# Kernel optimization log

Hardware: AMD Instinct MI355X
Metric: run time of the kernel (lower is better)

Reference implementation:

```python
import jax, jax.numpy as jnp
import numpy as np

N = 1_000_000
D_IN = 9      # 4 (pe) + 1 (q) + 4 (s)
D_H = 30      # dim_evolution
D_OUT = 1     # dim
SLOPE = 0.01  # torch LeakyReLU default negative_slope


def setup_inputs() -> dict:
    key = jax.random.key(0)
    ks = jax.random.split(key, 11)
    def lin(kw, kb, fan_in, fan_out):
        bound = 1.0 / np.sqrt(fan_in)
        W = jax.random.uniform(kw, (fan_in, fan_out), jnp.float32, -bound, bound)
        b = jax.random.uniform(kb, (fan_out,), jnp.float32, -bound, bound)
        return W, b
    W1, b1 = lin(ks[0], ks[1], D_IN, D_H)
    W2, b2 = lin(ks[2], ks[3], D_H, D_H)
    W3, b3 = lin(ks[4], ks[5], D_H, D_H)
    W4, b4 = lin(ks[6], ks[7], D_H, D_OUT)
    return {
        "input_pe": jax.random.normal(ks[8], (N, 4), jnp.float32),
        "input_q": jax.random.normal(ks[9], (N, 1), jnp.float32),
        "input_s": jax.random.normal(ks[10], (N, 4), jnp.float32),
        "W1": W1, "b1": b1, "W2": W2, "b2": b2,
        "W3": W3, "b3": b3, "W4": W4, "b4": b4,
    }


def reference(input_pe, input_q, input_s, W1, b1, W2, b2, W3, b3, W4, b4):
    # forward MLP 9->30->30->30->1 with LeakyReLU
    x = jnp.concatenate([input_pe, input_q, input_s], axis=1)  # [N,9]
    z1 = x @ W1 + b1
    h1 = jnp.where(z1 > 0, z1, SLOPE * z1)
    z2 = h1 @ W2 + b2
    h2 = jnp.where(z2 > 0, z2, SLOPE * z2)
    z3 = h2 @ W3 + b3
    h3 = jnp.where(z3 > 0, z3, SLOPE * z3)
    out = h3 @ W4 + b4  # [N,1]

    # analytic per-sample gradient of scalar output wrt the 9 inputs
    # (equivalent to torch.autograd.grad with grad_outputs=ones)
    gz3 = W4[:, 0][None, :] * jnp.where(z3 > 0, 1.0, SLOPE)  # [N,30]
    gz2 = (gz3 @ W3.T) * jnp.where(z2 > 0, 1.0, SLOPE)       # [N,30]
    gz1 = (gz2 @ W2.T) * jnp.where(z1 > 0, 1.0, SLOPE)       # [N,30]
    gx = gz1 @ W1.T                                           # [N,9]

    n = x.shape[0]
    h_pe = gx[:, 0:4].reshape(n, 1, 4)
    h_q = gx[:, 4:5].reshape(n, 1, 1)
    h_s = gx[:, 5:9].reshape(n, 1, 4)
    return (out, h_s, h_q, h_pe)
```

## Files before the change

### kernel.cpp

```cpp
#include <hip/hip_runtime.h>

#define DH 30
#define SLOPE 0.01f

typedef float v2 __attribute__((ext_vector_type(2)));
#define SB() __builtin_amdgcn_sched_barrier(0)

#define W1_OFF 0
#define W2_OFF 288
#define W3_OFF 1248
#define B1_OFF 2208
#define B2_OFF 2240
#define B3_OFF 2272
#define W4_OFF 2304
#define B4_OFF 2336

__global__ __launch_bounds__(256, 3) void mlp_fwdbwd(
    const float4* __restrict__ pe,
    const float*  __restrict__ q,
    const float4* __restrict__ s,
    const float* __restrict__ W1, const float* __restrict__ b1,
    const float* __restrict__ W2, const float* __restrict__ b2,
    const float* __restrict__ W3, const float* __restrict__ b3,
    const float* __restrict__ W4, const float* __restrict__ b4,
    float* __restrict__ dout, int n)
{
    __shared__ float lw[2368];
    const int tid = threadIdx.x;
    for (int idx = tid; idx < 2368; idx += 256) {
        float v = 0.f;
        if (idx < 288)        { int tt = idx,        r = tt >> 5, c = tt & 31; v = (c < DH) ? W1[r * DH + c] : 0.f; }
        else if (idx < 1248)  { int tt = idx - 288,  r = tt >> 5, c = tt & 31; v = (c < DH) ? W2[r * DH + c] : 0.f; }
        else if (idx < 2208)  { int tt = idx - 1248, r = tt >> 5, c = tt & 31; v = (c < DH) ? W3[r * DH + c] : 0.f; }
        else if (idx < 2240)  { int c = idx - 2208; v = (c < DH) ? b1[c] : 0.f; }
        else if (idx < 2272)  { int c = idx - 2240; v = (c < DH) ? b2[c] : 0.f; }
        else if (idx < 2304)  { int c = idx - 2272; v = (c < DH) ? b3[c] : 0.f; }
        else if (idx < 2336)  { int c = idx - 2304; v = (c < DH) ? W4[c] : 0.f; }
        else if (idx == 2336) { v = b4[0]; }
        lw[idx] = v;
    }
    __syncthreads();

    const int i = blockIdx.x * 256 + tid;
    if (i >= n) return;

    const float4 vpe = pe[i];
    const float4 vs  = s[i];
    const float  vq  = q[i];
    float x[9] = { vpe.x, vpe.y, vpe.z, vpe.w, vq, vs.x, vs.y, vs.z, vs.w };

    v2 acc[15];
    v2 hh[15];
    unsigned m1 = 0, m2 = 0, m3 = 0;
    const v2 slope2 = { SLOPE, SLOPE };

    #define ROW_FMA(OFF, k, sv)                                               \
    {                                                                         \
        const float4* Wr4 = reinterpret_cast<const float4*>(lw + OFF + (k)*32);\
        const v2*     Wr2 = reinterpret_cast<const v2*>(lw + OFF + (k)*32);   \
        _Pragma("unroll")                                                     \
        for (int j4 = 0; j4 < 7; ++j4) {                                      \
            const float4 w = Wr4[j4];                                         \
            const v2 wlo = { w.x, w.y };                                      \
            const v2 whi = { w.z, w.w };                                      \
            acc[2*j4]   = __builtin_elementwise_fma(sv, wlo, acc[2*j4]);      \
            acc[2*j4+1] = __builtin_elementwise_fma(sv, whi, acc[2*j4+1]);    \
        }                                                                     \
        acc[14] = __builtin_elementwise_fma(sv, Wr2[14], acc[14]);            \
    }

    #pragma unroll
    for (int jj = 0; jj < 15; ++jj) acc[jj] = (v2){0.f, 0.f};
    #pragma unroll
    for (int k = 0; k < 9; ++k) {
        const v2 xv = { x[k], x[k] };
        ROW_FMA(W1_OFF, k, xv);
        SB();
    }
    {
        const v2* bv = reinterpret_cast<const v2*>(lw + B1_OFF);
        #pragma unroll
        for (int jj = 0; jj < 15; ++jj) {
            const v2 z = acc[jj] + bv[jj];
            if (z.x > 0.f) m1 |= (1u << (2*jj));
            if (z.y > 0.f) m1 |= (1u << (2*jj+1));
            hh[jj] = __builtin_elementwise_max(z, z * slope2);
        }
    }
    SB();

    #pragma unroll
    for (int jj = 0; jj < 15; ++jj) acc[jj] = (v2){0.f, 0.f};
    #pragma unroll
    for (int k = 0; k < DH; ++k) {
        const float hk = hh[k >> 1][k & 1];
        const v2 hv = { hk, hk };
        ROW_FMA(W2_OFF, k, hv);
        SB();
    }
    {
        const v2* bv = reinterpret_cast<const v2*>(lw + B2_OFF);
        #pragma unroll
        for (int jj = 0; jj < 15; ++jj) {
            const v2 z = acc[jj] + bv[jj];
            if (z.x > 0.f) m2 |= (1u << (2*jj));
            if (z.y > 0.f) m2 |= (1u << (2*jj+1));
            hh[jj] = __builtin_elementwise_max(z, z * slope2);
        }
    }
    SB();

    #pragma unroll
    for (int jj = 0; jj < 15; ++jj) acc[jj] = (v2){0.f, 0.f};
    #pragma unroll
    for (int k = 0; k < DH; ++k) {
        const float hk = hh[k >> 1][k & 1];
        const v2 hv = { hk, hk };
        ROW_FMA(W3_OFF, k, hv);
        SB();
    }
    const float* b3p = lw + B3_OFF;
    const float* W4p = lw + W4_OFF;
    float outv = 0.f;
    #pragma unroll
    for (int j = 0; j < DH; ++j) {
        const float z = acc[j >> 1][j & 1] + b3p[j];
        if (z > 0.f) m3 |= (1u << j);
        const float hz = (z > 0.f) ? z : SLOPE * z;
        outv = fmaf(hz, W4p[j], outv);
    }
    outv += lw[B4_OFF];
    SB();

    v2 g3[15];
    {
        const v2* w4v = reinterpret_cast<const v2*>(W4p);
        #pragma unroll
        for (int jj = 0; jj < 15; ++jj) {
            const v2 w = w4v[jj];
            g3[jj].x = ((m3 >> (2*jj))   & 1u) ? w.x : SLOPE * w.x;
            g3[jj].y = ((m3 >> (2*jj+1)) & 1u) ? w.y : SLOPE * w.y;
        }
    }
    #define ROW_DOT(OFF, k, G, D)                                             \
    {                                                                         \
        const float4* Wr4 = reinterpret_cast<const float4*>(lw + OFF + (k)*32);\
        const v2*     Wr2 = reinterpret_cast<const v2*>(lw + OFF + (k)*32);   \
        v2 da = (v2){0.f, 0.f}, db = (v2){0.f, 0.f};                          \
        _Pragma("unroll")                                                     \
        for (int j4 = 0; j4 < 7; ++j4) {                                      \
            const float4 w = Wr4[j4];                                         \
            const v2 wlo = { w.x, w.y };                                      \
            const v2 whi = { w.z, w.w };                                      \
            da = __builtin_elementwise_fma(G[2*j4],   wlo, da);               \
            db = __builtin_elementwise_fma(G[2*j4+1], whi, db);               \
        }                                                                     \
        da = __builtin_elementwise_fma(G[14], Wr2[14], da);                   \
        D = (da.x + da.y) + (db.x + db.y);                                    \
    }

    v2 g2[15];
    #pragma unroll
    for (int k = 0; k < DH; ++k) {
        float dot;
        ROW_DOT(W3_OFF, k, g3, dot);
        g2[k >> 1][k & 1] = ((m2 >> k) & 1u) ? dot : SLOPE * dot;
        SB();
    }
    v2 g1[15];
    #pragma unroll
    for (int k = 0; k < DH; ++k) {
        float dot;
        ROW_DOT(W2_OFF, k, g2, dot);
        g1[k >> 1][k & 1] = ((m1 >> k) & 1u) ? dot : SLOPE * dot;
        SB();
    }
    float gx[9];
    #pragma unroll
    for (int k = 0; k < 9; ++k) {
        float dot;
        ROW_DOT(W1_OFF, k, g1, dot);
        gx[k] = dot;
        SB();
    }

    dout[i] = outv;
    float4* hs = reinterpret_cast<float4*>(dout + (size_t)n);
    hs[i] = make_float4(gx[5], gx[6], gx[7], gx[8]);
    dout[(size_t)5 * n + i] = gx[4];
    float4* hpe = reinterpret_cast<float4*>(dout + (size_t)6 * n);
    hpe[i] = make_float4(gx[0], gx[1], gx[2], gx[3]);
}

extern "C" void kernel_launch(void* const* d_in, const int* in_sizes, int n_in,
                              void* d_out, int out_size, void* d_ws, size_t ws_size,
                              hipStream_t stream) {
    const int n = in_sizes[1];
    const int blocks = (n + 255) / 256;
    hipLaunchKernelGGL(mlp_fwdbwd, dim3(blocks), dim3(256), 0, stream,
        (const float4*)d_in[0], (const float*)d_in[1], (const float4*)d_in[2],
        (const float*)d_in[3], (const float*)d_in[4],
        (const float*)d_in[5], (const float*)d_in[6],
        (const float*)d_in[7], (const float*)d_in[8],
        (const float*)d_in[9], (const float*)d_in[10],
        (float*)d_out, n);
}
```

Baseline: 153.8 us.

## Read backward-pass weights directly from global memory as uniform scalar loads

```diff
diff --git a/kernel.cpp b/kernel.cpp
--- a/kernel.cpp
+++ b/kernel.cpp
@@ -134,54 +134,45 @@
 
     v2 g3[15];
     {
-        const v2* w4v = reinterpret_cast<const v2*>(W4p);
         #pragma unroll
         for (int jj = 0; jj < 15; ++jj) {
-            const v2 w = w4v[jj];
-            g3[jj].x = ((m3 >> (2*jj))   & 1u) ? w.x : SLOPE * w.x;
-            g3[jj].y = ((m3 >> (2*jj+1)) & 1u) ? w.y : SLOPE * w.y;
+            const float wx = W4[2*jj];
+            const float wy = W4[2*jj+1];
+            g3[jj].x = ((m3 >> (2*jj))   & 1u) ? wx : SLOPE * wx;
+            g3[jj].y = ((m3 >> (2*jj+1)) & 1u) ? wy : SLOPE * wy;
         }
     }
-    #define ROW_DOT(OFF, k, G, D)                                             \
-    {                                                                         \
-        const float4* Wr4 = reinterpret_cast<const float4*>(lw + OFF + (k)*32);\
-        const v2*     Wr2 = reinterpret_cast<const v2*>(lw + OFF + (k)*32);   \
-        v2 da = (v2){0.f, 0.f}, db = (v2){0.f, 0.f};                          \
-        _Pragma("unroll")                                                     \
-        for (int j4 = 0; j4 < 7; ++j4) {                                      \
-            const float4 w = Wr4[j4];                                         \
-            const v2 wlo = { w.x, w.y };                                      \
-            const v2 whi = { w.z, w.w };                                      \
-            da = __builtin_elementwise_fma(G[2*j4],   wlo, da);               \
-            db = __builtin_elementwise_fma(G[2*j4+1], whi, db);               \
-        }                                                                     \
-        da = __builtin_elementwise_fma(G[14], Wr2[14], da);                   \
-        D = (da.x + da.y) + (db.x + db.y);                                    \
-    }
-
     v2 g2[15];
     #pragma unroll
     for (int k = 0; k < DH; ++k) {
-        float dot;
-        ROW_DOT(W3_OFF, k, g3, dot);
+        v2 d = (v2){0.f, 0.f};
+        const v2* Wr = reinterpret_cast<const v2*>(W3 + k * DH);
+        #pragma unroll
+        for (int jj = 0; jj < 15; ++jj)
+            d = __builtin_elementwise_fma(g3[jj], Wr[jj], d);
+        const float dot = d.x + d.y;
         g2[k >> 1][k & 1] = ((m2 >> k) & 1u) ? dot : SLOPE * dot;
-        SB();
     }
     v2 g1[15];
     #pragma unroll
     for (int k = 0; k < DH; ++k) {
-        float dot;
-        ROW_DOT(W2_OFF, k, g2, dot);
+        v2 d = (v2){0.f, 0.f};
+        const v2* Wr = reinterpret_cast<const v2*>(W2 + k * DH);
+        #pragma unroll
+        for (int jj = 0; jj < 15; ++jj)
+            d = __builtin_elementwise_fma(g2[jj], Wr[jj], d);
+        const float dot = d.x + d.y;
         g1[k >> 1][k & 1] = ((m1 >> k) & 1u) ? dot : SLOPE * dot;
-        SB();
     }
     float gx[9];
     #pragma unroll
     for (int k = 0; k < 9; ++k) {
-        float dot;
-        ROW_DOT(W1_OFF, k, g1, dot);
-        gx[k] = dot;
-        SB();
+        v2 d = (v2){0.f, 0.f};
+        const v2* Wr = reinterpret_cast<const v2*>(W1 + k * DH);
+        #pragma unroll
+        for (int jj = 0; jj < 15; ++jj)
+            d = __builtin_elementwise_fma(g1[jj], Wr[jj], d);
+        gx[k] = d.x + d.y;
     }
 
     dout[i] = outv;
```

Result: faster. 134.2 us (-12.8%).
